# Kernel optimization log

Measured on AMD Instinct MI355X. Metric: run time of the kernel, lower is better.

Reference implementation:

```python
import math
import jax, jax.numpy as jnp
import numpy as np

# ---------- real Wigner 3j (e3nn convention, unit Frobenius norm) ----------
def _su2_cg(j1, j2, j3):
    def f(n):
        return math.factorial(round(n))
    mat = np.zeros((2 * j1 + 1, 2 * j2 + 1, 2 * j3 + 1))
    for m1 in range(-j1, j1 + 1):
        for m2 in range(-j2, j2 + 1):
            m3 = m1 + m2
            if abs(m3) > j3:
                continue
            vmin = max(-j1 + j2 + m3, -j1 + m1, 0)
            vmax = min(j2 + j3 + m1, j3 - j1 + j2, j3 + m3)
            C = math.sqrt((2 * j3 + 1) * f(j3 + j1 - j2) * f(j3 - j1 + j2) * f(j1 + j2 - j3)
                          * f(j3 + m3) * f(j3 - m3)
                          / (f(j1 + j2 + j3 + 1) * f(j1 - m1) * f(j1 + m1) * f(j2 - m2) * f(j2 + m2)))
            S = 0.0
            for v in range(vmin, vmax + 1):
                S += (-1) ** (v + j2 + m2) * f(j2 + j3 + m1 - v) * f(j1 - m1 + v) / (
                    f(v) * f(j3 - j1 + j2 - v) * f(j3 + m3 - v) * f(v + j1 - j2 - m3))
            mat[j1 + m1, j2 + m2, j3 + m3] = C * S
    return mat

def _real_to_complex(l):
    q = np.zeros((2 * l + 1, 2 * l + 1), dtype=np.complex128)
    for m in range(-l, 0):
        q[l + m, l + abs(m)] = 1.0 / math.sqrt(2)
        q[l + m, l - abs(m)] = -1j / math.sqrt(2)
    q[l, l] = 1.0
    for m in range(1, l + 1):
        q[l + m, l + abs(m)] = (-1) ** m / math.sqrt(2)
        q[l + m, l - abs(m)] = 1j * (-1) ** m / math.sqrt(2)
    return (-1j) ** l * q

def _wigner_3j(l1, l2, l3):
    Q1, Q2, Q3 = _real_to_complex(l1), _real_to_complex(l2), _real_to_complex(l3)
    C = _su2_cg(l1, l2, l3).astype(np.complex128)
    C = np.einsum('ij,kl,mn,ikn->jlm', Q1, Q2, np.conj(Q3.T), C).real
    return (C / np.linalg.norm(C)).astype(np.float32)

# ---------- architecture constants (from init_kwargs) ----------
IRREPS_NODE = [(128, 0), (64, 1), (32, 2)]   # 128x0e+64x1e+32x2e, dim 480
IRREPS_EDGE = [(1, 0), (1, 1), (1, 2)]       # 1x0e+1x1e+1x2e (spherical harmonics), dim 9
OUT_LS = (0, 1, 2)
N_NODES, N_EDGES, N_BASIS = 10000, 80000, 128
FC_HIDDEN = 64
AVG_AGG = 8.0
NODE_DIM = sum(m * (2 * l + 1) for m, l in IRREPS_NODE)  # 480

# uvu instructions: (i, l1, j, l2, l3, mul); kept if ir_out in output irreps or 0e
INSTRUCTIONS = []
for _i, (_mul, _l1) in enumerate(IRREPS_NODE):
    for _j, (_, _l2) in enumerate(IRREPS_EDGE):
        for _l3 in range(abs(_l1 - _l2), _l1 + _l2 + 1):
            if _l3 in OUT_LS:
                INSTRUCTIONS.append((_i, _l1, _j, _l2, _l3, _mul))
WEIGHT_NUMEL = sum(ins[5] for ins in INSTRUCTIONS)                       # 960
CAT_MULS = {l: sum(ins[5] for ins in INSTRUCTIONS if ins[4] == l) for l in OUT_LS}  # {0:224,1:384,2:352}
W3J = {(l1, l2, l3): jnp.asarray(_wigner_3j(l1, l2, l3))
       for (_, l1, _, l2, l3, _) in INSTRUCTIONS}

def _layernorm(x, g, b):
    mu = jnp.mean(x, axis=-1, keepdims=True)
    var = jnp.mean((x - mu) ** 2, axis=-1, keepdims=True)
    return (x - mu) * jax.lax.rsqrt(var + 1e-5) * g + b

def _forward(node_input, edge_attr, edge_scalars, edge_src, edge_dst,
             exp_w, exp_b, rad_w1, rad_b1, rad_ln1_g, rad_ln1_b,
             rad_w2, rad_b2, rad_ln2_g, rad_ln2_b, rad_w3, rad_offset,
             proj_w0, proj_w1, proj_w2, proj_b):
    N = node_input.shape[0]
    E = edge_attr.shape[0]
    dt = node_input.dtype
    # exp: LinearRS('1x0e' -> irreps) applied to all-ones scalars; only 0e channels populated
    node0 = jnp.broadcast_to(exp_w + exp_b, (N, IRREPS_NODE[0][0]))   # [N,128]
    xs = [node0[edge_src][:, :, None],                                # [E,128,1] gather by edge_src
          jnp.zeros((E, IRREPS_NODE[1][0], 3), dt),                   # 1e block (structurally zero)
          jnp.zeros((E, IRREPS_NODE[2][0], 5), dt)]                   # 2e block (structurally zero)
    ys = [edge_attr[:, 0:1], edge_attr[:, 1:4], edge_attr[:, 4:9]]
    # radial MLP -> per-edge TP weights [E, 960]
    h = jax.nn.silu(_layernorm(edge_scalars @ rad_w1 + rad_b1, rad_ln1_g, rad_ln1_b))
    h = jax.nn.silu(_layernorm(h @ rad_w2 + rad_b2, rad_ln2_g, rad_ln2_b))
    w = h @ rad_w3 + rad_offset
    # depthwise ('uvu') CG tensor product, outputs grouped by l (even-first sort; all even here)
    per_l = {l: [] for l in OUT_LS}
    off = 0
    for (i, l1, j, l2, l3, mul) in INSTRUCTIONS:
        w_ins = w[:, off:off + mul]   # [E, mul] (v = 1)
        off += mul
        cg = W3J[(l1, l2, l3)] * math.sqrt(2 * l3 + 1)
        per_l[l3].append(jnp.einsum('ijk,eui,ej,eu->euk', cg, xs[i], ys[j], w_ins))
    cat = {l: jnp.concatenate(per_l[l], axis=1) for l in OUT_LS}      # [E, CAT_MULS[l], 2l+1]
    # proj: e3nn Linear (per-l multiplicity mixing; bias on scalars only)
    p0 = jnp.einsum('eui,uo->eoi', cat[0], proj_w0) + proj_b[None, :, None]
    p1 = jnp.einsum('eui,uo->eoi', cat[1], proj_w1)
    p2 = jnp.einsum('eui,uo->eoi', cat[2], proj_w2)
    edge_feat = jnp.concatenate([p0.reshape(E, -1), p1.reshape(E, -1), p2.reshape(E, -1)], axis=1)  # [E,480]
    # scaled scatter-add over destination nodes
    out = jax.ops.segment_sum(edge_feat, edge_dst, num_segments=N)
    return out / math.sqrt(AVG_AGG)

def setup_inputs() -> dict:
    key = jax.random.key(0)
    ks = jax.random.split(key, 16)
    f32 = jnp.float32
    inv = lambda n: 1.0 / math.sqrt(n)
    return {
        'node_input': jax.random.normal(ks[0], (N_NODES, NODE_DIM), f32),
        'edge_attr': jax.random.normal(ks[1], (N_EDGES, 9), f32),
        'edge_scalars': jax.random.uniform(ks[2], (N_EDGES, N_BASIS), f32),
        'edge_src': jax.random.randint(ks[3], (N_EDGES,), 0, N_NODES),
        'edge_dst': jax.random.randint(ks[4], (N_EDGES,), 0, N_NODES),
        'batch': jnp.zeros((N_NODES,), jnp.int32),
        'exp_w': jax.random.normal(ks[5], (128,), f32),
        'exp_b': jnp.zeros((128,), f32),
        'rad_w1': jax.random.normal(ks[6], (N_BASIS, FC_HIDDEN), f32) * inv(N_BASIS),
        'rad_b1': jnp.zeros((FC_HIDDEN,), f32),
        'rad_ln1_g': jnp.ones((FC_HIDDEN,), f32),
        'rad_ln1_b': jnp.zeros((FC_HIDDEN,), f32),
        'rad_w2': jax.random.normal(ks[7], (FC_HIDDEN, FC_HIDDEN), f32) * inv(FC_HIDDEN),
        'rad_b2': jnp.zeros((FC_HIDDEN,), f32),
        'rad_ln2_g': jnp.ones((FC_HIDDEN,), f32),
        'rad_ln2_b': jnp.zeros((FC_HIDDEN,), f32),
        'rad_w3': jax.random.normal(ks[8], (FC_HIDDEN, WEIGHT_NUMEL), f32) * inv(FC_HIDDEN),
        'rad_offset': jax.random.normal(ks[9], (WEIGHT_NUMEL,), f32) * 0.1,
        'proj_w0': jax.random.normal(ks[10], (CAT_MULS[0], 128), f32) * inv(CAT_MULS[0]),
        'proj_w1': jax.random.normal(ks[11], (CAT_MULS[1], 64), f32) * inv(CAT_MULS[1]),
        'proj_w2': jax.random.normal(ks[12], (CAT_MULS[2], 32), f32) * inv(CAT_MULS[2]),
        'proj_b': jnp.zeros((128,), f32),
    }

def reference(node_input, edge_attr, edge_scalars, edge_src, edge_dst, batch,
              exp_w, exp_b, rad_w1, rad_b1, rad_ln1_g, rad_ln1_b,
              rad_w2, rad_b2, rad_ln2_g, rad_ln2_b, rad_w3, rad_offset,
              proj_w0, proj_w1, proj_w2, proj_b):
    return _forward(node_input, edge_attr, edge_scalars, edge_src, edge_dst,
                    exp_w, exp_b, rad_w1, rad_b1, rad_ln1_g, rad_ln1_b,
                    rad_w2, rad_b2, rad_ln2_g, rad_ln2_b, rad_w3, rad_offset,
                    proj_w0, proj_w1, proj_w2, proj_b)
```

## Files before the change

### kernel.cpp

```cpp
#include <hip/hip_runtime.h>
#include <math.h>


#define NEDGES 80000
#define NNODES 10000

__device__ __forceinline__ float readlane_f(float v, int l) {
    return __builtin_bit_cast(float, __builtin_amdgcn_readlane(__builtin_bit_cast(int, v), l));
}
__device__ __forceinline__ float silu_f(float y) {
    return y / (1.0f + __expf(-y));
}

__global__ __launch_bounds__(256) void precompute_and_hist(
    const float* __restrict__ exp_w, const float* __restrict__ exp_b,
    const float* __restrict__ rad_w3,
    const float* __restrict__ rad_offset,
    const float* __restrict__ proj_w0,
    const float* __restrict__ proj_w1,
    const float* __restrict__ proj_w2,
    float* __restrict__ M, float* __restrict__ cvec,
    const int* __restrict__ edge_dst, int* __restrict__ counts)
{
    if (blockIdx.x >= 65) {
        int b = blockIdx.x - 65;
        for (int e = b * 256 + threadIdx.x; e < NEDGES; e += 100 * 256)
            atomicAdd(&counts[edge_dst[e]], 1);
        return;
    }
    __shared__ float x0[128];
    int t = threadIdx.x;
    if (t < 128) x0[t] = exp_w[t] + exp_b[t];
    __syncthreads();
    if (t >= 224) return;
    int h = blockIdx.x;
    const float* src = (h < 64) ? (rad_w3 + h * 960) : rad_offset;
    float acc = 0.0f;
    if (t < 128) {
#pragma unroll 4
        for (int u = 0; u < 128; ++u) acc += src[u] * x0[u] * proj_w0[u * 128 + t];
    } else if (t < 192) {
        int o = t - 128;
#pragma unroll 4
        for (int u = 0; u < 128; ++u) acc += src[128 + u] * x0[u] * proj_w1[u * 64 + o];
    } else {
        int o = t - 192;
#pragma unroll 4
        for (int u = 0; u < 128; ++u) acc += src[256 + u] * x0[u] * proj_w2[u * 32 + o];
    }
    if (h < 64) M[h * 224 + t] = acc;
    else        cvec[t] = acc;
}

__global__ __launch_bounds__(1024) void scan_counts(
    int* __restrict__ counts,
    int* __restrict__ offsets)
{
    __shared__ int wsum[16];
    const int t = threadIdx.x;
    const int lane = t & 63, w = t >> 6;
    const int base = t * 10;
    int local[10];
    int s = 0;
#pragma unroll
    for (int i = 0; i < 10; ++i) {
        int idx = base + i;
        int v = (idx < NNODES) ? counts[idx] : 0;
        local[i] = s;
        s += v;
    }
    int incl = s;
#pragma unroll
    for (int off = 1; off < 64; off <<= 1) {
        int up = __shfl_up(incl, off, 64);
        if (lane >= off) incl += up;
    }
    if (lane == 63) wsum[w] = incl;
    __syncthreads();
    if (t < 16) {
        int v = wsum[t];
#pragma unroll
        for (int off = 1; off < 16; off <<= 1) {
            int up = __shfl_up(v, off, 64);
            if (t >= off) v += up;
        }
        wsum[t] = v;
    }
    __syncthreads();
    int wbase = (w == 0) ? 0 : wsum[w - 1];
    int excl = wbase + incl - s;
#pragma unroll
    for (int i = 0; i < 10; ++i) {
        int idx = base + i;
        if (idx < NNODES) {
            offsets[idx] = excl + local[i];
            counts[idx] = 0;
        }
    }
    if (t == 1023) offsets[NNODES] = excl + s;
}

__global__ __launch_bounds__(256) void edge_h2(
    const float* __restrict__ edge_scalars,
    const int*   __restrict__ edge_dst,
    const int*   __restrict__ offsets,
    int*         __restrict__ cursor,
    const float* __restrict__ rad_w1,
    const float* __restrict__ rad_b1,
    const float* __restrict__ g1, const float* __restrict__ bt1,
    const float* __restrict__ rad_w2,
    const float* __restrict__ rad_b2,
    const float* __restrict__ g2, const float* __restrict__ bt2,
    float* __restrict__ h2csr,
    int*   __restrict__ order)
{
    __shared__ float S[16384 + 64];
    float* W1s = S;
    float* W2s = S + 8192;
    float* ES  = S + 12288;
    int*   pos_s = (int*)(S + 16384);

    const int t    = threadIdx.x;
    const int lane = t & 63;
    const int wid  = t >> 6;
    const int er   = lane & 3;
    const int cc   = lane >> 2;
    const int eb   = blockIdx.x * 64;

    {
        const float4* s1 = (const float4*)rad_w1;
        float4* d1 = (float4*)W1s;
#pragma unroll
        for (int i = 0; i < 8; ++i) d1[t + i * 256] = s1[t + i * 256];
        const float4* s2 = (const float4*)rad_w2;
        float4* d2 = (float4*)W2s;
#pragma unroll
        for (int i = 0; i < 4; ++i) d2[t + i * 256] = s2[t + i * 256];
    }
    if (t < 64) {
        int e = eb + t;
        int d = edge_dst[e];
        int p = offsets[d] + atomicAdd(&cursor[d], 1);
        order[p] = e;
        pos_s[t] = p;
    }
    {
        const int re = t >> 2, seg = t & 3;
        const float* row = edge_scalars + (size_t)(eb + re) * 128;
#pragma unroll
        for (int q = 0; q < 4; ++q) {
            float4 v = *(const float4*)(row + seg * 16 + q * 4);
            ES[(seg * 16 + q * 4 + 0) * 64 + re] = v.x;
            ES[(seg * 16 + q * 4 + 1) * 64 + re] = v.y;
            ES[(seg * 16 + q * 4 + 2) * 64 + re] = v.z;
            ES[(seg * 16 + q * 4 + 3) * 64 + re] = v.w;
        }
    }
    __syncthreads();

    const int n0 = cc * 4;
    float b1v[4], g1v[4], t1v[4], b2v[4], g2v[4], t2v[4];
#pragma unroll
    for (int j = 0; j < 4; ++j) {
        b1v[j] = rad_b1[n0 + j]; g1v[j] = g1[n0 + j]; t1v[j] = bt1[n0 + j];
        b2v[j] = rad_b2[n0 + j]; g2v[j] = g2[n0 + j]; t2v[j] = bt2[n0 + j];
    }

    float acc[4][4];
#pragma unroll
    for (int i = 0; i < 4; ++i)
#pragma unroll
        for (int j = 0; j < 4; ++j) acc[i][j] = b1v[j];

    const int ecol = wid * 16 + er * 4;

#pragma unroll 8
    for (int k = 0; k < 64; ++k) {
        float4 av = *(const float4*)&ES[k * 64 + ecol];
        float4 wv = *(const float4*)&W1s[k * 64 + n0];
        float a4[4] = {av.x, av.y, av.z, av.w};
        float w4[4] = {wv.x, wv.y, wv.z, wv.w};
#pragma unroll
        for (int i = 0; i < 4; ++i)
#pragma unroll
            for (int j = 0; j < 4; ++j) acc[i][j] = fmaf(a4[i], w4[j], acc[i][j]);
    }
    __syncthreads();
    {
        const int re = t >> 2, seg = t & 3;
        const float* row = edge_scalars + (size_t)(eb + re) * 128 + 64;
#pragma unroll
        for (int q = 0; q < 4; ++q) {
            float4 v = *(const float4*)(row + seg * 16 + q * 4);
            ES[(seg * 16 + q * 4 + 0) * 64 + re] = v.x;
            ES[(seg * 16 + q * 4 + 1) * 64 + re] = v.y;
            ES[(seg * 16 + q * 4 + 2) * 64 + re] = v.z;
            ES[(seg * 16 + q * 4 + 3) * 64 + re] = v.w;
        }
    }
    __syncthreads();
#pragma unroll 8
    for (int k = 0; k < 64; ++k) {
        float4 av = *(const float4*)&ES[k * 64 + ecol];
        float4 wv = *(const float4*)&W1s[(64 + k) * 64 + n0];
        float a4[4] = {av.x, av.y, av.z, av.w};
        float w4[4] = {wv.x, wv.y, wv.z, wv.w};
#pragma unroll
        for (int i = 0; i < 4; ++i)
#pragma unroll
            for (int j = 0; j < 4; ++j) acc[i][j] = fmaf(a4[i], w4[j], acc[i][j]);
    }
    __syncthreads();

    float* H = W1s + wid * 1280;
    {
        float s1i[4], s2i[4];
#pragma unroll
        for (int i = 0; i < 4; ++i) {
            s1i[i] = acc[i][0] + acc[i][1] + acc[i][2] + acc[i][3];
            s2i[i] = acc[i][0] * acc[i][0] + acc[i][1] * acc[i][1]
                   + acc[i][2] * acc[i][2] + acc[i][3] * acc[i][3];
        }
#pragma unroll
        for (int m = 4; m <= 32; m <<= 1) {
#pragma unroll
            for (int i = 0; i < 4; ++i) {
                s1i[i] += __shfl_xor(s1i[i], m, 64);
                s2i[i] += __shfl_xor(s2i[i], m, 64);
            }
        }
#pragma unroll
        for (int i = 0; i < 4; ++i) {
            float mu  = s1i[i] * (1.0f / 64.0f);
            float var = s2i[i] * (1.0f / 64.0f) - mu * mu;
            float rs  = rsqrtf(var + 1e-5f);
#pragma unroll
            for (int j = 0; j < 4; ++j) {
                float y = (acc[i][j] - mu) * rs * g1v[j] + t1v[j];
                H[(n0 + j) * 20 + er * 4 + i] = silu_f(y);
            }
        }
    }

    float acc2[4][4];
#pragma unroll
    for (int i = 0; i < 4; ++i)
#pragma unroll
        for (int j = 0; j < 4; ++j) acc2[i][j] = b2v[j];
#pragma unroll 8
    for (int u = 0; u < 64; ++u) {
        float4 hv = *(const float4*)&H[u * 20 + er * 4];
        float4 wv = *(const float4*)&W2s[u * 64 + n0];
        float h4[4] = {hv.x, hv.y, hv.z, hv.w};
        float w4[4] = {wv.x, wv.y, wv.z, wv.w};
#pragma unroll
        for (int i = 0; i < 4; ++i)
#pragma unroll
            for (int j = 0; j < 4; ++j) acc2[i][j] = fmaf(h4[i], w4[j], acc2[i][j]);
    }

    {
        float s1i[4], s2i[4];
#pragma unroll
        for (int i = 0; i < 4; ++i) {
            s1i[i] = acc2[i][0] + acc2[i][1] + acc2[i][2] + acc2[i][3];
            s2i[i] = acc2[i][0] * acc2[i][0] + acc2[i][1] * acc2[i][1]
                   + acc2[i][2] * acc2[i][2] + acc2[i][3] * acc2[i][3];
        }
#pragma unroll
        for (int m = 4; m <= 32; m <<= 1) {
#pragma unroll
            for (int i = 0; i < 4; ++i) {
                s1i[i] += __shfl_xor(s1i[i], m, 64);
                s2i[i] += __shfl_xor(s2i[i], m, 64);
            }
        }
#pragma unroll
        for (int i = 0; i < 4; ++i) {
            float mu  = s1i[i] * (1.0f / 64.0f);
            float var = s2i[i] * (1.0f / 64.0f) - mu * mu;
            float rs  = rsqrtf(var + 1e-5f);
            float4 v;
            v.x = silu_f((acc2[i][0] - mu) * rs * g2v[0] + t2v[0]);
            v.y = silu_f((acc2[i][1] - mu) * rs * g2v[1] + t2v[1]);
            v.z = silu_f((acc2[i][2] - mu) * rs * g2v[2] + t2v[2]);
            v.w = silu_f((acc2[i][3] - mu) * rs * g2v[3] + t2v[3]);
            *(float4*)&ES[(wid * 16 + er * 4 + i) * 64 + n0] = v;
        }
    }
    __syncthreads();

    {
        const int r = t >> 2, p = t & 3;
        int pos = pos_s[r];
        float* dst = h2csr + (size_t)pos * 64 + p * 16;
        const float* src = &ES[r * 64 + p * 16];
#pragma unroll
        for (int q = 0; q < 4; ++q)
            *(float4*)(dst + q * 4) = *(const float4*)(src + q * 4);
    }
}

__global__ __launch_bounds__(1024) void node_gather(
    const float* __restrict__ h2csr,
    const float* __restrict__ edge_attr,
    const int*   __restrict__ order,
    const int*   __restrict__ offsets,
    const float* __restrict__ M,
    const float* __restrict__ cvec,
    const float* __restrict__ proj_b,
    float* __restrict__ out)
{
    __shared__ float ldsM[64 * 224];
    for (int i = threadIdx.x; i < 64 * 224; i += 1024) ldsM[i] = M[i];
    __syncthreads();

    const int lane = threadIdx.x & 63;
    const int n = __builtin_amdgcn_readfirstlane(blockIdx.x * 16 + (threadIdx.x >> 6));
    const int s0 = offsets[n], s1 = offsets[n + 1];

    float T[9]  = {0, 0, 0, 0, 0, 0, 0, 0, 0};
    float ys[9] = {0, 0, 0, 0, 0, 0, 0, 0, 0};
    for (int i = s0; i < s1; ++i) {
        float hv = h2csr[(size_t)i * 64 + lane];
        int e = order[i];
        const float* ya = edge_attr + (size_t)e * 9;
#pragma unroll
        for (int k = 0; k < 9; ++k) {
            float y = ya[k];
            T[k] += hv * y;
            ys[k] += y;
        }
    }

    const int l32 = lane & 31;
    float acc0a = 0.0f, acc0b = 0.0f;
    float acc1[3] = {0, 0, 0};
    float acc2[5] = {0, 0, 0, 0, 0};
#pragma unroll 4
    for (int u = 0; u < 64; ++u) {
        const float* Mu = ldsM + u * 224;
        float m0a = Mu[lane];
        float m0b = Mu[64 + lane];
        float m1  = Mu[128 + lane];
        float m2  = Mu[192 + l32];
        float t0 = readlane_f(T[0], u);
        acc0a += m0a * t0;
        acc0b += m0b * t0;
#pragma unroll
        for (int k = 0; k < 3; ++k) acc1[k] += m1 * readlane_f(T[1 + k], u);
#pragma unroll
        for (int k = 0; k < 5; ++k) acc2[k] += m2 * readlane_f(T[4 + k], u);
    }

    constexpr float inv_s8 = 0.35355339059327373f;
    const float cnt = (float)(s1 - s0);
    float* ob = out + (size_t)n * 480;
    ob[lane]      = (acc0a + cvec[lane] * ys[0]      + cnt * proj_b[lane])      * inv_s8;
    ob[64 + lane] = (acc0b + cvec[64 + lane] * ys[0] + cnt * proj_b[64 + lane]) * inv_s8;
#pragma unroll
    for (int k = 0; k < 3; ++k)
        ob[128 + lane * 3 + k] = (acc1[k] + cvec[128 + lane] * ys[1 + k]) * inv_s8;
    if (lane < 32) {
#pragma unroll
        for (int k = 0; k < 5; ++k)
            ob[320 + lane * 5 + k] = (acc2[k] + cvec[192 + lane] * ys[4 + k]) * inv_s8;
    }
}

extern "C" void kernel_launch(void* const* d_in, const int* in_sizes, int n_in,
                              void* d_out, int out_size, void* d_ws, size_t ws_size,
                              hipStream_t stream)
{
    const float* edge_attr    = (const float*)d_in[1];
    const float* edge_scalars = (const float*)d_in[2];
    const int*   edge_dst     = (const int*)d_in[4];
    const float* exp_w   = (const float*)d_in[6];
    const float* exp_b   = (const float*)d_in[7];
    const float* rad_w1  = (const float*)d_in[8];
    const float* rad_b1  = (const float*)d_in[9];
    const float* g1      = (const float*)d_in[10];
    const float* bt1     = (const float*)d_in[11];
    const float* rad_w2  = (const float*)d_in[12];
    const float* rad_b2  = (const float*)d_in[13];
    const float* g2      = (const float*)d_in[14];
    const float* bt2     = (const float*)d_in[15];
    const float* rad_w3  = (const float*)d_in[16];
    const float* rad_off = (const float*)d_in[17];
    const float* pw0     = (const float*)d_in[18];
    const float* pw1     = (const float*)d_in[19];
    const float* pw2     = (const float*)d_in[20];
    const float* proj_b  = (const float*)d_in[21];

    float* M       = (float*)d_ws;
    float* cvec    = M + 64 * 224;
    float* h2csr   = cvec + 224;
    int*   counts  = (int*)(h2csr + (size_t)NEDGES * 64);
    int*   offsets = counts + NNODES;
    int*   order   = offsets + NNODES + 1;

    hipMemsetAsync(counts, 0, NNODES * sizeof(int), stream);
    precompute_and_hist<<<165, 256, 0, stream>>>(exp_w, exp_b, rad_w3, rad_off,
        pw0, pw1, pw2, M, cvec, edge_dst, counts);
    scan_counts<<<1, 1024, 0, stream>>>(counts, offsets);
    edge_h2<<<NEDGES / 64, 256, 0, stream>>>(edge_scalars, edge_dst,
        offsets, counts, rad_w1, rad_b1, g1, bt1, rad_w2, rad_b2, g2, bt2,
        h2csr, order);
    node_gather<<<NNODES / 16, 1024, 0, stream>>>(h2csr, edge_attr, order,
        offsets, M, cvec, proj_b, (float*)d_out);
}
```

Measured before the change: 121.4 us.

## Split node gather into T-build pass and register-tiled projection GEMM kernel

The fused node_gather kernel, which did a per-node projection with readlane broadcasts, is split into two kernels. t_build accumulates per-node T and ys sums into a global buffer. proj then runs a register-tiled, LDS-staged GEMM over blocks of nodes, with separate block ranges for the l=0, l=1 and l=2 outputs. This replaces the serial readlane-bound inner loop with a dense tiled matmul, at the cost of an extra global round trip of about 23 MB for Tbuf and one more kernel launch.

```diff
diff --git a/kernel.cpp b/kernel.cpp
--- a/kernel.cpp
+++ b/kernel.cpp
@@ -4,10 +4,10 @@
 
 #define NEDGES 80000
 #define NNODES 10000
-
-__device__ __forceinline__ float readlane_f(float v, int l) {
-    return __builtin_bit_cast(float, __builtin_amdgcn_readlane(__builtin_bit_cast(int, v), l));
-}
+#define NPAD   10048
+#define NB_L0  157
+#define NB_L12 313
+
 __device__ __forceinline__ float silu_f(float y) {
     return y / (1.0f + __expf(-y));
 }
@@ -53,8 +53,7 @@
 }
 
 __global__ __launch_bounds__(1024) void scan_counts(
-    int* __restrict__ counts,
-    int* __restrict__ offsets)
+    int* __restrict__ counts, int* __restrict__ offsets)
 {
     __shared__ int wsum[16];
     const int t = threadIdx.x;
@@ -301,70 +300,225 @@
     }
 }
 
-__global__ __launch_bounds__(1024) void node_gather(
+__global__ __launch_bounds__(1024) void t_build(
     const float* __restrict__ h2csr,
     const float* __restrict__ edge_attr,
     const int*   __restrict__ order,
+    const int*   __restrict__ offsets,
+    float* __restrict__ Tbuf,
+    float* __restrict__ ysb)
+{
+    const int lane = threadIdx.x & 63;
+    const int n = __builtin_amdgcn_readfirstlane(blockIdx.x * 16 + (threadIdx.x >> 6));
+    const int s0 = offsets[n], s1 = offsets[n + 1];
+
+    float T[9]  = {0, 0, 0, 0, 0, 0, 0, 0, 0};
+    float ys[9] = {0, 0, 0, 0, 0, 0, 0, 0, 0};
+    for (int i = s0; i < s1; ++i) {
+        float hv = h2csr[(size_t)i * 64 + lane];
+        int e = order[i];
+        const float* ya = edge_attr + (size_t)e * 9;
+#pragma unroll
+        for (int k = 0; k < 9; ++k) {
+            float y = ya[k];
+            T[k] += hv * y;
+            ys[k] += y;
+        }
+    }
+    float* tb = Tbuf + (size_t)n * 576;
+#pragma unroll
+    for (int k = 0; k < 9; ++k) tb[k * 64 + lane] = T[k];
+#pragma unroll
+    for (int k = 0; k < 9; ++k) if (lane == k) ysb[n * 9 + k] = ys[k];
+}
+
+__global__ __launch_bounds__(256) void proj(
+    const float* __restrict__ Tbuf, const float* __restrict__ ysb,
     const int*   __restrict__ offsets,
     const float* __restrict__ M,
     const float* __restrict__ cvec,
     const float* __restrict__ proj_b,
     float* __restrict__ out)
 {
-    __shared__ float ldsM[64 * 224];
-    for (int i = threadIdx.x; i < 64 * 224; i += 1024) ldsM[i] = M[i];
-    __syncthreads();
-
-    const int lane = threadIdx.x & 63;
-    const int n = __builtin_amdgcn_readfirstlane(blockIdx.x * 16 + (threadIdx.x >> 6));
-    const int s0 = offsets[n], s1 = offsets[n + 1];
-
-    float T[9]  = {0, 0, 0, 0, 0, 0, 0, 0, 0};
-    float ys[9] = {0, 0, 0, 0, 0, 0, 0, 0, 0};
-    for (int i = s0; i < s1; ++i) {
-        float hv = h2csr[(size_t)i * 64 + lane];
-        int e = order[i];
-        const float* ya = edge_attr + (size_t)e * 9;
-#pragma unroll
-        for (int k = 0; k < 9; ++k) {
-            float y = ya[k];
-            T[k] += hv * y;
-            ys[k] += y;
-        }
-    }
-
-    const int l32 = lane & 31;
-    float acc0a = 0.0f, acc0b = 0.0f;
-    float acc1[3] = {0, 0, 0};
-    float acc2[5] = {0, 0, 0, 0, 0};
+    __shared__ float S[13248];
+    const int tid = threadIdx.x;
+    const int bid = blockIdx.x;
+    constexpr float inv = 0.35355339059327373f;
+
+    if (bid < NB_L0) {
+        const int n0 = bid * 64;
+        for (int it = tid; it < 1024; it += 256) {
+            int ni = it >> 4, q4 = it & 15;
+            float4 v = *(const float4*)&Tbuf[(size_t)(n0 + ni) * 576 + q4 * 4];
+            S[(q4 * 4 + 0) * 66 + ni] = v.x;
+            S[(q4 * 4 + 1) * 66 + ni] = v.y;
+            S[(q4 * 4 + 2) * 66 + ni] = v.z;
+            S[(q4 * 4 + 3) * 66 + ni] = v.w;
+        }
+        for (int it = tid; it < 2048; it += 256) {
+            int u = it >> 5, c4 = it & 31;
+            *(float4*)&S[4224 + u * 128 + c4 * 4] = *(const float4*)&M[u * 224 + c4 * 4];
+        }
+        __syncthreads();
+        const int np = tid & 15, cg = tid >> 4;
+        float acc[4][8];
+#pragma unroll
+        for (int i = 0; i < 4; ++i)
+#pragma unroll
+            for (int j = 0; j < 8; ++j) acc[i][j] = 0.0f;
 #pragma unroll 4
-    for (int u = 0; u < 64; ++u) {
-        const float* Mu = ldsM + u * 224;
-        float m0a = Mu[lane];
-        float m0b = Mu[64 + lane];
-        float m1  = Mu[128 + lane];
-        float m2  = Mu[192 + l32];
-        float t0 = readlane_f(T[0], u);
-        acc0a += m0a * t0;
-        acc0b += m0b * t0;
-#pragma unroll
-        for (int k = 0; k < 3; ++k) acc1[k] += m1 * readlane_f(T[1 + k], u);
-#pragma unroll
-        for (int k = 0; k < 5; ++k) acc2[k] += m2 * readlane_f(T[4 + k], u);
-    }
-
-    constexpr float inv_s8 = 0.35355339059327373f;
-    const float cnt = (float)(s1 - s0);
-    float* ob = out + (size_t)n * 480;
-    ob[lane]      = (acc0a + cvec[lane] * ys[0]      + cnt * proj_b[lane])      * inv_s8;
-    ob[64 + lane] = (acc0b + cvec[64 + lane] * ys[0] + cnt * proj_b[64 + lane]) * inv_s8;
-#pragma unroll
-    for (int k = 0; k < 3; ++k)
-        ob[128 + lane * 3 + k] = (acc1[k] + cvec[128 + lane] * ys[1 + k]) * inv_s8;
-    if (lane < 32) {
-#pragma unroll
-        for (int k = 0; k < 5; ++k)
-            ob[320 + lane * 5 + k] = (acc2[k] + cvec[192 + lane] * ys[4 + k]) * inv_s8;
+        for (int u = 0; u < 64; ++u) {
+            float4 tv = *(const float4*)&S[u * 66 + np * 4];
+            float4 m0 = *(const float4*)&S[4224 + u * 128 + cg * 8];
+            float4 m1 = *(const float4*)&S[4224 + u * 128 + cg * 8 + 4];
+            float ta[4] = {tv.x, tv.y, tv.z, tv.w};
+            float ma[8] = {m0.x, m0.y, m0.z, m0.w, m1.x, m1.y, m1.z, m1.w};
+#pragma unroll
+            for (int i = 0; i < 4; ++i)
+#pragma unroll
+                for (int j = 0; j < 8; ++j) acc[i][j] = fmaf(ta[i], ma[j], acc[i][j]);
+        }
+#pragma unroll
+        for (int i = 0; i < 4; ++i) {
+            int n = n0 + np * 4 + i;
+            if (n >= NNODES) continue;
+            float ys0 = ysb[n * 9];
+            float cnt = (float)(offsets[n + 1] - offsets[n]);
+            float f[8];
+#pragma unroll
+            for (int j = 0; j < 8; ++j) {
+                int col = cg * 8 + j;
+                f[j] = (acc[i][j] + cvec[col] * ys0 + cnt * proj_b[col]) * inv;
+            }
+            *(float4*)&out[(size_t)n * 480 + cg * 8]     = *(float4*)&f[0];
+            *(float4*)&out[(size_t)n * 480 + cg * 8 + 4] = *(float4*)&f[4];
+        }
+    } else if (bid < NB_L0 + NB_L12) {
+        const int n0 = (bid - NB_L0) * 32;
+        for (int it = tid; it < 1536; it += 256) {
+            int r = it >> 4, q4 = it & 15;
+            int kq = r >> 5, ni = r & 31;
+            float4 v = *(const float4*)&Tbuf[(size_t)(n0 + ni) * 576 + (1 + kq) * 64 + q4 * 4];
+            float* dst = &S[kq * 2176];
+            dst[(q4 * 4 + 0) * 34 + ni] = v.x;
+            dst[(q4 * 4 + 1) * 34 + ni] = v.y;
+            dst[(q4 * 4 + 2) * 34 + ni] = v.z;
+            dst[(q4 * 4 + 3) * 34 + ni] = v.w;
+        }
+        for (int it = tid; it < 1024; it += 256) {
+            int u = it >> 4, c4 = it & 15;
+            *(float4*)&S[6528 + u * 64 + c4 * 4] = *(const float4*)&M[u * 224 + 128 + c4 * 4];
+        }
+        __syncthreads();
+        const int np = tid & 15, cg = tid >> 4;
+        float acc[2][4][3];
+#pragma unroll
+        for (int i = 0; i < 2; ++i)
+#pragma unroll
+            for (int j = 0; j < 4; ++j)
+#pragma unroll
+                for (int kq = 0; kq < 3; ++kq) acc[i][j][kq] = 0.0f;
+#pragma unroll 4
+        for (int u = 0; u < 64; ++u) {
+            float2 t0 = *(const float2*)&S[0 * 2176 + u * 34 + np * 2];
+            float2 t1 = *(const float2*)&S[1 * 2176 + u * 34 + np * 2];
+            float2 t2 = *(const float2*)&S[2 * 2176 + u * 34 + np * 2];
+            float4 m  = *(const float4*)&S[6528 + u * 64 + cg * 4];
+            float ma[4] = {m.x, m.y, m.z, m.w};
+            float ta[2][3] = {{t0.x, t1.x, t2.x}, {t0.y, t1.y, t2.y}};
+#pragma unroll
+            for (int i = 0; i < 2; ++i)
+#pragma unroll
+                for (int j = 0; j < 4; ++j) {
+                    acc[i][j][0] = fmaf(ta[i][0], ma[j], acc[i][j][0]);
+                    acc[i][j][1] = fmaf(ta[i][1], ma[j], acc[i][j][1]);
+                    acc[i][j][2] = fmaf(ta[i][2], ma[j], acc[i][j][2]);
+                }
+        }
+#pragma unroll
+        for (int i = 0; i < 2; ++i) {
+            int n = n0 + np * 2 + i;
+            if (n >= NNODES) continue;
+            float y1 = ysb[n * 9 + 1], y2 = ysb[n * 9 + 2], y3 = ysb[n * 9 + 3];
+            float f[12];
+#pragma unroll
+            for (int j = 0; j < 4; ++j) {
+                int cc = cg * 4 + j;
+                float cv = cvec[128 + cc];
+                f[j * 3 + 0] = (acc[i][j][0] + cv * y1) * inv;
+                f[j * 3 + 1] = (acc[i][j][1] + cv * y2) * inv;
+                f[j * 3 + 2] = (acc[i][j][2] + cv * y3) * inv;
+            }
+            float* dst = &out[(size_t)n * 480 + 128 + cg * 12];
+            *(float4*)(dst + 0) = *(float4*)&f[0];
+            *(float4*)(dst + 4) = *(float4*)&f[4];
+            *(float4*)(dst + 8) = *(float4*)&f[8];
+        }
+    } else {
+        const int n0 = (bid - NB_L0 - NB_L12) * 32;
+        for (int it = tid; it < 2560; it += 256) {
+            int r = it >> 4, q4 = it & 15;
+            int kq = r >> 5, ni = r & 31;
+            float4 v = *(const float4*)&Tbuf[(size_t)(n0 + ni) * 576 + (4 + kq) * 64 + q4 * 4];
+            float* dst = &S[kq * 2176];
+            dst[(q4 * 4 + 0) * 34 + ni] = v.x;
+            dst[(q4 * 4 + 1) * 34 + ni] = v.y;
+            dst[(q4 * 4 + 2) * 34 + ni] = v.z;
+            dst[(q4 * 4 + 3) * 34 + ni] = v.w;
+        }
+        for (int it = tid; it < 512; it += 256) {
+            int u = it >> 3, c4 = it & 7;
+            *(float4*)&S[10880 + u * 32 + c4 * 4] = *(const float4*)&M[u * 224 + 192 + c4 * 4];
+        }
+        __syncthreads();
+        const int np = tid & 15, cg = tid >> 4;
+        float acc[2][2][5];
+#pragma unroll
+        for (int i = 0; i < 2; ++i)
+#pragma unroll
+            for (int j = 0; j < 2; ++j)
+#pragma unroll
+                for (int kq = 0; kq < 5; ++kq) acc[i][j][kq] = 0.0f;
+#pragma unroll 4
+        for (int u = 0; u < 64; ++u) {
+            float2 tq[5];
+#pragma unroll
+            for (int kq = 0; kq < 5; ++kq)
+                tq[kq] = *(const float2*)&S[kq * 2176 + u * 34 + np * 2];
+            float2 m = *(const float2*)&S[10880 + u * 32 + cg * 2];
+            float ma[2] = {m.x, m.y};
+#pragma unroll
+            for (int i = 0; i < 2; ++i) {
+                float ti[5] = {(&tq[0].x)[i], (&tq[1].x)[i], (&tq[2].x)[i],
+                               (&tq[3].x)[i], (&tq[4].x)[i]};
+#pragma unroll
+                for (int j = 0; j < 2; ++j)
+#pragma unroll
+                    for (int kq = 0; kq < 5; ++kq)
+                        acc[i][j][kq] = fmaf(ti[kq], ma[j], acc[i][j][kq]);
+            }
+        }
+#pragma unroll
+        for (int i = 0; i < 2; ++i) {
+            int n = n0 + np * 2 + i;
+            if (n >= NNODES) continue;
+            float yk[5];
+#pragma unroll
+            for (int kq = 0; kq < 5; ++kq) yk[kq] = ysb[n * 9 + 4 + kq];
+            float f[10];
+#pragma unroll
+            for (int j = 0; j < 2; ++j) {
+                int cc = cg * 2 + j;
+                float cv = cvec[192 + cc];
+#pragma unroll
+                for (int kq = 0; kq < 5; ++kq)
+                    f[j * 5 + kq] = (acc[i][j][kq] + cv * yk[kq]) * inv;
+            }
+            float* dst = &out[(size_t)n * 480 + 320 + cg * 10];
+#pragma unroll
+            for (int q = 0; q < 5; ++q)
+                *(float2*)(dst + q * 2) = *(float2*)&f[q * 2];
+        }
     }
 }
 
@@ -393,11 +547,13 @@
     const float* proj_b  = (const float*)d_in[21];
 
     float* M       = (float*)d_ws;
-    float* cvec    = M + 64 * 224;
+    float* cvec    = M + 14336;
     float* h2csr   = cvec + 224;
     int*   counts  = (int*)(h2csr + (size_t)NEDGES * 64);
     int*   offsets = counts + NNODES;
     int*   order   = offsets + NNODES + 1;
+    float* Tbuf    = (float*)(order + NEDGES);
+    float* ysb     = Tbuf + (size_t)NPAD * 576;
 
     hipMemsetAsync(counts, 0, NNODES * sizeof(int), stream);
     precompute_and_hist<<<165, 256, 0, stream>>>(exp_w, exp_b, rad_w3, rad_off,
@@ -406,6 +562,8 @@
     edge_h2<<<NEDGES / 64, 256, 0, stream>>>(edge_scalars, edge_dst,
         offsets, counts, rad_w1, rad_b1, g1, bt1, rad_w2, rad_b2, g2, bt2,
         h2csr, order);
-    node_gather<<<NNODES / 16, 1024, 0, stream>>>(h2csr, edge_attr, order,
-        offsets, M, cvec, proj_b, (float*)d_out);
-}
+    t_build<<<NNODES / 16, 1024, 0, stream>>>(h2csr, edge_attr, order,
+        offsets, Tbuf, ysb);
+    proj<<<NB_L0 + 2 * NB_L12, 256, 0, stream>>>(Tbuf, ysb, offsets,
+        M, cvec, proj_b, (float*)d_out);
+}
```

Result: faster. 112.1 us (-7.6%).
